# Performance work log

Hardware: AMD Instinct MI355X
Metric: run time of the kernel (lower is better)

Reference implementation:

```python
import jax, jax.numpy as jnp
import numpy as np

B, S, D, F, E, TOP_K = 4, 1024, 512, 2048, 16, 2
TEMPERATURE = 0.5
STD = 0.02


def setup_inputs() -> dict:
    key = jax.random.key(0)
    ks = jax.random.split(key, 9)
    f32 = jnp.float32
    return {
        "x": jax.random.normal(ks[0], (B, S, D), f32),
        # router gate: Linear(D, D//2) -> ReLU -> Linear(D//2, E)
        "gate_w1": jax.random.normal(ks[1], (D, D // 2), f32) * STD,
        "gate_b1": jnp.zeros((D // 2,), f32),
        "gate_w2": jax.random.normal(ks[2], (D // 2, E), f32) * STD,
        "gate_b2": jnp.zeros((E,), f32),
        # stacked expert weights (E experts, each D->F->D)
        "up_w": jax.random.normal(ks[3], (E, D, F), f32) * STD,
        "up_b": jnp.zeros((E, F), f32),
        "down_w": jax.random.normal(ks[4], (E, F, D), f32) * STD,
        "down_b": jnp.zeros((E, D), f32),
    }


def reference(x, gate_w1, gate_b1, gate_w2, gate_b2, up_w, up_b, down_w, down_b):
    num_experts = up_w.shape[0]
    # ---- router ----
    h = jax.nn.relu(x @ gate_w1 + gate_b1)                      # [B,S,D//2]
    scores = h @ gate_w2 + gate_b2                              # [B,S,E]
    routing_probs = jax.nn.softmax(scores / TEMPERATURE, axis=-1)
    # load-balance loss: MSE(mean usage, uniform)
    batch_usage = routing_probs.mean(axis=(0, 1))               # [E]
    load_balance_loss = jnp.mean((batch_usage - 1.0 / num_experts) ** 2)
    # ---- top-k routing weights, renormalized via softmax over selected scores ----
    top_vals, top_idx = jax.lax.top_k(routing_probs, TOP_K)     # [B,S,K]
    top_probs = jax.nn.softmax(top_vals, axis=-1)               # [B,S,K]
    # scatter per-token top-k probs into dense [B,S,E] combine weights
    expert_probs = jnp.einsum(
        "bske,bsk->bse", jax.nn.one_hot(top_idx, num_experts, dtype=x.dtype), top_probs
    )
    # ---- every expert computed densely on all tokens, masked combine (faithful to source) ----
    hid = jax.nn.gelu(
        jnp.einsum("bsd,edf->ebsf", x, up_w) + up_b[:, None, None, :],
        approximate=False,
    )                                                            # [E,B,S,F]
    expert_out = jnp.einsum("ebsf,efd->ebsd", hid, down_w) + down_b[:, None, None, :]
    output = jnp.einsum("ebsd,bse->bsd", expert_out, expert_probs)  # [B,S,D]
    return output, load_balance_loss, routing_probs
```

## Files before the change

### kernel.cpp

```cpp
#include <hip/hip_runtime.h>
#include <hip/hip_bf16.h>

#define NTOK 4096
#define DIM  512
#define DH   256
#define NE   16
#define FF   2048
#define CAP  8192
#define MAXTILES 80
#define TEMP_INV 2.0f

#define OUT_LOSS  (NTOK * DIM)
#define OUT_PROBS (NTOK * DIM + 1)

#define WS_CNT    0
#define WS_USAGE  64
#define WS_NTILES 128
#define WS_DESC   256
#define WS_WTS    1024
#define WS_LISTS  36864
#define WS_HID    (1u << 20)
#define WS_PAIR   (48u << 20)

typedef __attribute__((ext_vector_type(8))) short bf16x8;
typedef __attribute__((ext_vector_type(8))) unsigned short u16x8;
typedef __attribute__((ext_vector_type(4))) float f32x4;

__device__ __forceinline__ unsigned short f2bf(float f) {
  union { float f; unsigned u; } c; c.f = f;
  return (unsigned short)((c.u + 0x7FFFu + ((c.u >> 16) & 1u)) >> 16);
}
__device__ __forceinline__ float gc(const float4& v, int c) {
  return c == 0 ? v.x : c == 1 ? v.y : c == 2 ? v.z : v.w;
}

__launch_bounds__(256)
__global__ void router_kernel(const float* __restrict__ x,
                              const float* __restrict__ w1,
                              const float* __restrict__ b1,
                              const float* __restrict__ w2,
                              const float* __restrict__ b2,
                              float* __restrict__ out,
                              int* __restrict__ cnt,
                              float* __restrict__ usage,
                              float* __restrict__ wts,
                              int* __restrict__ lists) {
  __shared__ __align__(16) float xs[16][DIM];
  __shared__ __align__(16) float hs[16][DH + 4];
  __shared__ __align__(16) float w2s[DH * NE];
  __shared__ float ps[16][NE];

  int tid = threadIdx.x;
  int tok0 = blockIdx.x * 16;

  {
    const float4* xg = (const float4*)(x + (size_t)tok0 * DIM);
    float4* xv = (float4*)&xs[0][0];
    for (int i = tid; i < 16 * DIM / 4; i += 256) xv[i] = xg[i];
    for (int i = tid; i < DH * NE; i += 256) w2s[i] = w2[i];
  }
  __syncthreads();

  {
    int j = tid;
    float acc[16];
    float bj = b1[j];
#pragma unroll
    for (int t = 0; t < 16; ++t) acc[t] = bj;
    for (int k = 0; k < DIM; k += 4) {
      float wa = w1[(k + 0) * DH + j];
      float wb = w1[(k + 1) * DH + j];
      float wcv = w1[(k + 2) * DH + j];
      float wd = w1[(k + 3) * DH + j];
#pragma unroll
      for (int t = 0; t < 16; ++t) {
        float4 xv = *(const float4*)&xs[t][k];
        acc[t] = fmaf(xv.x, wa, acc[t]);
        acc[t] = fmaf(xv.y, wb, acc[t]);
        acc[t] = fmaf(xv.z, wcv, acc[t]);
        acc[t] = fmaf(xv.w, wd, acc[t]);
      }
    }
#pragma unroll
    for (int t = 0; t < 16; ++t) hs[t][j] = fmaxf(acc[t], 0.f);
  }
  __syncthreads();

  int t = tid >> 4, e = tid & 15;
  float s = b2[e];
  for (int j = 0; j < DH; ++j) s = fmaf(hs[t][j], w2s[j * NE + e], s);
  s *= TEMP_INV;
  float m = s;
#pragma unroll
  for (int d = 1; d < 16; d <<= 1) m = fmaxf(m, __shfl_xor(m, d));
  float p = expf(s - m);
  float sum = p;
#pragma unroll
  for (int d = 1; d < 16; d <<= 1) sum += __shfl_xor(sum, d);
  float prob = p / sum;
  out[OUT_PROBS + (size_t)(tok0 + t) * NE + e] = prob;
  ps[t][e] = prob;

  float v = prob;
  v += __shfl_xor(v, 16);
  v += __shfl_xor(v, 32);
  if ((tid & 63) < 16) atomicAdd(&usage[e], v);
  __syncthreads();

  if (tid < 16) {
    int tt = tid;
    float v1 = -1.f; int i1 = 0;
    for (int ee = 0; ee < NE; ++ee) { float pv = ps[tt][ee]; if (pv > v1) { v1 = pv; i1 = ee; } }
    float v2 = -1.f; int i2 = 0;
    for (int ee = 0; ee < NE; ++ee) { if (ee == i1) continue; float pv = ps[tt][ee]; if (pv > v2) { v2 = pv; i2 = ee; } }
    float mm = fmaxf(v1, v2);
    float e0 = expf(v1 - mm), e1 = expf(v2 - mm);
    float rs = 1.f / (e0 + e1);
    int gt = tok0 + tt;
    wts[2 * gt]     = e0 * rs;
    wts[2 * gt + 1] = e1 * rs;
    int p1 = atomicAdd(&cnt[i1], 1);
    lists[i1 * CAP + p1] = 2 * gt;
    int p2 = atomicAdd(&cnt[i2], 1);
    lists[i2 * CAP + p2] = 2 * gt + 1;
  }
}

__global__ void sched_kernel(const int* __restrict__ cnt,
                             const float* __restrict__ usage,
                             int* __restrict__ ntiles,
                             int2* __restrict__ desc,
                             float* __restrict__ out_loss) {
  if (threadIdx.x == 0) {
    int n = 0;
    for (int e = 0; e < NE; ++e) {
      int c = cnt[e];
      for (int i = 0; i < c; i += 128) { desc[n] = make_int2(e, i); ++n; }
    }
    *ntiles = n;
    float loss = 0.f;
    for (int e = 0; e < NE; ++e) {
      float d = usage[e] * (1.f / 4096.f) - (1.f / 16.f);
      loss += d * d;
    }
    *out_loss = loss * (1.f / 16.f);
  }
}

__launch_bounds__(256)
__global__ void up_kernel(const float* __restrict__ x,
                          const float* __restrict__ up_w,
                          const float* __restrict__ up_b,
                          const int* __restrict__ cnt,
                          const int* __restrict__ ntiles,
                          const int2* __restrict__ desc,
                          const int* __restrict__ lists,
                          unsigned short* __restrict__ hid) {
  int ty = blockIdx.y;
  if (ty >= *ntiles) return;
  int2 dd = desc[ty];
  int e = dd.x, i0 = dd.y;
  int cntE = cnt[e];
  int f0 = blockIdx.x * 128;
  const float* __restrict__ W = up_w + (size_t)e * (DIM * FF);

  __shared__ __align__(16) unsigned short As[128 * 64];
  __shared__ __align__(16) unsigned short Bs[128 * 64];

  int tid = threadIdx.x;
  int ar = tid >> 1, ah = tid & 1;
  int aidx = i0 + ar;
  int aslot = (aidx < cntE) ? lists[e * CAP + aidx] : 0;
  const float* __restrict__ xrow = x + (size_t)(aslot >> 1) * DIM;

  int kk8 = tid >> 5;
  int n4 = (tid & 31) << 2;

  int lane = tid & 63, wid = tid >> 6;
  int wr = wid >> 1, wc = wid & 1;
  int ln15 = lane & 15, lq = lane >> 4;

  f32x4 acc[4][4];
#pragma unroll
  for (int i = 0; i < 4; ++i)
#pragma unroll
    for (int j = 0; j < 4; ++j) acc[i][j] = f32x4{0.f, 0.f, 0.f, 0.f};

  for (int ks = 0; ks < DIM / 64; ++ks) {
    int k0 = ks * 64;
#pragma unroll
    for (int i = 0; i < 4; ++i) {
      int g = (ah << 2) + i;
      float4 u = *(const float4*)(xrow + k0 + g * 8);
      float4 w = *(const float4*)(xrow + k0 + g * 8 + 4);
      u16x8 pk;
      pk[0] = f2bf(u.x); pk[1] = f2bf(u.y); pk[2] = f2bf(u.z); pk[3] = f2bf(u.w);
      pk[4] = f2bf(w.x); pk[5] = f2bf(w.y); pk[6] = f2bf(w.z); pk[7] = f2bf(w.w);
      *(u16x8*)(As + ar * 64 + ((g ^ (ar & 7)) << 3)) = pk;
    }
    float4 bw[8];
#pragma unroll
    for (int rr = 0; rr < 8; ++rr)
      bw[rr] = *(const float4*)(W + (size_t)(k0 + kk8 * 8 + rr) * FF + f0 + n4);
#pragma unroll
    for (int c = 0; c < 4; ++c) {
      int n = n4 + c;
      u16x8 pk;
#pragma unroll
      for (int rr = 0; rr < 8; ++rr) pk[rr] = f2bf(gc(bw[rr], c));
      *(u16x8*)(Bs + n * 64 + ((kk8 ^ (n & 7)) << 3)) = pk;
    }
    __syncthreads();
#pragma unroll
    for (int ksub = 0; ksub < 2; ++ksub) {
      bf16x8 a[4], b[4];
      int g = (ksub << 2) + lq;
#pragma unroll
      for (int mi = 0; mi < 4; ++mi) {
        int arow = (wr << 6) + (mi << 4) + ln15;
        a[mi] = *(const bf16x8*)(As + arow * 64 + ((g ^ (arow & 7)) << 3));
      }
#pragma unroll
      for (int ni = 0; ni < 4; ++ni) {
        int bcol = (wc << 6) + (ni << 4) + ln15;
        b[ni] = *(const bf16x8*)(Bs + bcol * 64 + ((g ^ (bcol & 7)) << 3));
      }
#pragma unroll
      for (int mi = 0; mi < 4; ++mi)
#pragma unroll
        for (int ni = 0; ni < 4; ++ni)
          acc[mi][ni] = __builtin_amdgcn_mfma_f32_16x16x32_bf16(a[mi], b[ni], acc[mi][ni], 0, 0, 0);
    }
    __syncthreads();
  }
#pragma unroll
  for (int mi = 0; mi < 4; ++mi) {
    int row_l = (wr << 6) + (mi << 4) + (lq << 2);
#pragma unroll
    for (int ni = 0; ni < 4; ++ni) {
      int col = (wc << 6) + (ni << 4) + ln15;
      float bias = up_b[e * FF + f0 + col];
#pragma unroll
      for (int q = 0; q < 4; ++q) {
        float vv = acc[mi][ni][q] + bias;
        float g = 0.5f * vv * (1.f + erff(vv * 0.70710678118f));
        hid[((size_t)ty * 128 + row_l + q) * FF + f0 + col] = f2bf(g);
      }
    }
  }
}

__launch_bounds__(256)
__global__ void down_kernel(const unsigned short* __restrict__ hid,
                            const float* __restrict__ down_w,
                            const float* __restrict__ down_b,
                            const int* __restrict__ cnt,
                            const int* __restrict__ ntiles,
                            const int2* __restrict__ desc,
                            const int* __restrict__ lists,
                            float* __restrict__ pairbuf) {
  int ty = blockIdx.y;
  if (ty >= *ntiles) return;
  int2 dd = desc[ty];
  int e = dd.x, i0 = dd.y;
  int cntE = cnt[e];
  int n0 = blockIdx.x * 128;
  const float* __restrict__ W = down_w + (size_t)e * (FF * DIM);

  __shared__ __align__(16) unsigned short As[128 * 64];
  __shared__ __align__(16) unsigned short Bs[128 * 64];

  int tid = threadIdx.x;
  int ar = tid >> 1, ah = tid & 1;
  const unsigned short* __restrict__ hrow = hid + ((size_t)ty * 128 + ar) * FF;

  int kk8 = tid >> 5;
  int n4 = (tid & 31) << 2;

  int lane = tid & 63, wid = tid >> 6;
  int wr = wid >> 1, wc = wid & 1;
  int ln15 = lane & 15, lq = lane >> 4;

  f32x4 acc[4][4];
#pragma unroll
  for (int i = 0; i < 4; ++i)
#pragma unroll
    for (int j = 0; j < 4; ++j) acc[i][j] = f32x4{0.f, 0.f, 0.f, 0.f};

  for (int ks = 0; ks < FF / 64; ++ks) {
    int k0 = ks * 64;
#pragma unroll
    for (int i = 0; i < 4; ++i) {
      int g = (ah << 2) + i;
      u16x8 pk = *(const u16x8*)(hrow + k0 + g * 8);
      *(u16x8*)(As + ar * 64 + ((g ^ (ar & 7)) << 3)) = pk;
    }
    float4 bw[8];
#pragma unroll
    for (int rr = 0; rr < 8; ++rr)
      bw[rr] = *(const float4*)(W + (size_t)(k0 + kk8 * 8 + rr) * DIM + n0 + n4);
#pragma unroll
    for (int c = 0; c < 4; ++c) {
      int n = n4 + c;
      u16x8 pk;
#pragma unroll
      for (int rr = 0; rr < 8; ++rr) pk[rr] = f2bf(gc(bw[rr], c));
      *(u16x8*)(Bs + n * 64 + ((kk8 ^ (n & 7)) << 3)) = pk;
    }
    __syncthreads();
#pragma unroll
    for (int ksub = 0; ksub < 2; ++ksub) {
      bf16x8 a[4], b[4];
      int g = (ksub << 2) + lq;
#pragma unroll
      for (int mi = 0; mi < 4; ++mi) {
        int arow = (wr << 6) + (mi << 4) + ln15;
        a[mi] = *(const bf16x8*)(As + arow * 64 + ((g ^ (arow & 7)) << 3));
      }
#pragma unroll
      for (int ni = 0; ni < 4; ++ni) {
        int bcol = (wc << 6) + (ni << 4) + ln15;
        b[ni] = *(const bf16x8*)(Bs + bcol * 64 + ((g ^ (bcol & 7)) << 3));
      }
#pragma unroll
      for (int mi = 0; mi < 4; ++mi)
#pragma unroll
        for (int ni = 0; ni < 4; ++ni)
          acc[mi][ni] = __builtin_amdgcn_mfma_f32_16x16x32_bf16(a[mi], b[ni], acc[mi][ni], 0, 0, 0);
    }
    __syncthreads();
  }
#pragma unroll
  for (int mi = 0; mi < 4; ++mi) {
    int row_l = (wr << 6) + (mi << 4) + (lq << 2);
#pragma unroll
    for (int ni = 0; ni < 4; ++ni) {
      int col = n0 + (wc << 6) + (ni << 4) + ln15;
      float bias = down_b[e * DIM + col];
#pragma unroll
      for (int q = 0; q < 4; ++q) {
        int idx = i0 + row_l + q;
        if (idx < cntE) {
          int slot = lists[e * CAP + idx];
          pairbuf[(size_t)slot * DIM + col] = acc[mi][ni][q] + bias;
        }
      }
    }
  }
}

__launch_bounds__(256)
__global__ void combine_kernel(const float* __restrict__ pairbuf,
                               const float* __restrict__ wts,
                               float* __restrict__ out) {
  int t = blockIdx.x;
  int d = threadIdx.x << 1;
  float w0 = wts[2 * t], w1 = wts[2 * t + 1];
  float2 a = *(const float2*)(pairbuf + (size_t)(2 * t) * DIM + d);
  float2 b = *(const float2*)(pairbuf + (size_t)(2 * t + 1) * DIM + d);
  float2 r; r.x = w0 * a.x + w1 * b.x; r.y = w0 * a.y + w1 * b.y;
  *(float2*)(out + (size_t)t * DIM + d) = r;
}

extern "C" void kernel_launch(void* const* d_in, const int* in_sizes, int n_in,
                              void* d_out, int out_size, void* d_ws, size_t ws_size,
                              hipStream_t stream) {
  (void)in_sizes; (void)n_in; (void)out_size; (void)ws_size;
  const float* x   = (const float*)d_in[0];
  const float* gw1 = (const float*)d_in[1];
  const float* gb1 = (const float*)d_in[2];
  const float* gw2 = (const float*)d_in[3];
  const float* gb2 = (const float*)d_in[4];
  const float* uw  = (const float*)d_in[5];
  const float* ub  = (const float*)d_in[6];
  const float* dw  = (const float*)d_in[7];
  const float* db  = (const float*)d_in[8];
  float* out = (float*)d_out;
  char* ws = (char*)d_ws;

  int*   cnt     = (int*)(ws + WS_CNT);
  float* usage   = (float*)(ws + WS_USAGE);
  int*   ntiles  = (int*)(ws + WS_NTILES);
  int2*  desc    = (int2*)(ws + WS_DESC);
  float* wts     = (float*)(ws + WS_WTS);
  int*   lists   = (int*)(ws + WS_LISTS);
  unsigned short* hid = (unsigned short*)(ws + WS_HID);
  float* pairbuf = (float*)(ws + WS_PAIR);

  hipMemsetAsync(d_ws, 0, 1024, stream);
  router_kernel<<<NTOK / 16, 256, 0, stream>>>(x, gw1, gb1, gw2, gb2, out, cnt, usage, wts, lists);
  sched_kernel<<<1, 64, 0, stream>>>(cnt, usage, ntiles, desc, out + OUT_LOSS);
  up_kernel<<<dim3(FF / 128, MAXTILES), 256, 0, stream>>>(x, uw, ub, cnt, ntiles, desc, lists, hid);
  down_kernel<<<dim3(DIM / 128, MAXTILES), 256, 0, stream>>>(hid, dw, db, cnt, ntiles, desc, lists, pairbuf);
  combine_kernel<<<NTOK, 256, 0, stream>>>(pairbuf, wts, out);
}
```

Baseline: 427.3 us.

## Halve router tokens per block, prefetch gate weights, parallelize scheduler scan

```diff
diff --git a/kernel.cpp b/kernel.cpp
--- a/kernel.cpp
+++ b/kernel.cpp
@@ -9,6 +9,7 @@
 #define CAP  8192
 #define MAXTILES 80
 #define TEMP_INV 2.0f
+#define RTOK 8
 
 #define OUT_LOSS  (NTOK * DIM)
 #define OUT_PROBS (NTOK * DIM + 1)
@@ -45,69 +46,88 @@
                               float* __restrict__ usage,
                               float* __restrict__ wts,
                               int* __restrict__ lists) {
-  __shared__ __align__(16) float xs[16][DIM];
-  __shared__ __align__(16) float hs[16][DH + 4];
+  __shared__ __align__(16) float xs[RTOK][DIM];
+  __shared__ __align__(16) float hs[RTOK][DH + 4];
   __shared__ __align__(16) float w2s[DH * NE];
-  __shared__ float ps[16][NE];
+  __shared__ float ps[RTOK][NE];
+  __shared__ float us[2][NE];
 
   int tid = threadIdx.x;
-  int tok0 = blockIdx.x * 16;
+  int tok0 = blockIdx.x * RTOK;
 
   {
     const float4* xg = (const float4*)(x + (size_t)tok0 * DIM);
     float4* xv = (float4*)&xs[0][0];
-    for (int i = tid; i < 16 * DIM / 4; i += 256) xv[i] = xg[i];
+    for (int i = tid; i < RTOK * DIM / 4; i += 256) xv[i] = xg[i];
     for (int i = tid; i < DH * NE; i += 256) w2s[i] = w2[i];
   }
   __syncthreads();
 
   {
     int j = tid;
-    float acc[16];
+    float acc[RTOK];
     float bj = b1[j];
 #pragma unroll
-    for (int t = 0; t < 16; ++t) acc[t] = bj;
-    for (int k = 0; k < DIM; k += 4) {
-      float wa = w1[(k + 0) * DH + j];
-      float wb = w1[(k + 1) * DH + j];
-      float wcv = w1[(k + 2) * DH + j];
-      float wd = w1[(k + 3) * DH + j];
-#pragma unroll
-      for (int t = 0; t < 16; ++t) {
-        float4 xv = *(const float4*)&xs[t][k];
-        acc[t] = fmaf(xv.x, wa, acc[t]);
-        acc[t] = fmaf(xv.y, wb, acc[t]);
-        acc[t] = fmaf(xv.z, wcv, acc[t]);
-        acc[t] = fmaf(xv.w, wd, acc[t]);
-      }
-    }
-#pragma unroll
-    for (int t = 0; t < 16; ++t) hs[t][j] = fmaxf(acc[t], 0.f);
+    for (int t = 0; t < RTOK; ++t) acc[t] = bj;
+
+    float wq[4][4];
+#pragma unroll
+    for (int g = 0; g < 4; ++g)
+#pragma unroll
+      for (int u = 0; u < 4; ++u)
+        wq[g][u] = w1[(size_t)(g * 4 + u) * DH + j];
+
+#pragma unroll 4
+    for (int g = 0; g < DIM / 4; ++g) {
+      float wcur[4];
+#pragma unroll
+      for (int u = 0; u < 4; ++u) wcur[u] = wq[g & 3][u];
+      int gn = g + 4;
+      if (gn < DIM / 4) {
+#pragma unroll
+        for (int u = 0; u < 4; ++u) wq[g & 3][u] = w1[(size_t)(gn * 4 + u) * DH + j];
+      }
+      int k = g * 4;
+#pragma unroll
+      for (int t = 0; t < RTOK; ++t) {
+        float4 xq = *(const float4*)&xs[t][k];
+        acc[t] = fmaf(xq.x, wcur[0], acc[t]);
+        acc[t] = fmaf(xq.y, wcur[1], acc[t]);
+        acc[t] = fmaf(xq.z, wcur[2], acc[t]);
+        acc[t] = fmaf(xq.w, wcur[3], acc[t]);
+      }
+    }
+#pragma unroll
+    for (int t = 0; t < RTOK; ++t) hs[t][j] = fmaxf(acc[t], 0.f);
   }
   __syncthreads();
 
   int t = tid >> 4, e = tid & 15;
-  float s = b2[e];
-  for (int j = 0; j < DH; ++j) s = fmaf(hs[t][j], w2s[j * NE + e], s);
-  s *= TEMP_INV;
-  float m = s;
-#pragma unroll
-  for (int d = 1; d < 16; d <<= 1) m = fmaxf(m, __shfl_xor(m, d));
-  float p = expf(s - m);
-  float sum = p;
-#pragma unroll
-  for (int d = 1; d < 16; d <<= 1) sum += __shfl_xor(sum, d);
-  float prob = p / sum;
-  out[OUT_PROBS + (size_t)(tok0 + t) * NE + e] = prob;
-  ps[t][e] = prob;
-
-  float v = prob;
-  v += __shfl_xor(v, 16);
-  v += __shfl_xor(v, 32);
-  if ((tid & 63) < 16) atomicAdd(&usage[e], v);
+  if (tid < 128) {
+    float s = b2[e];
+#pragma unroll 8
+    for (int jj = 0; jj < DH; ++jj) s = fmaf(hs[t][jj], w2s[jj * NE + e], s);
+    s *= TEMP_INV;
+    float m = s;
+#pragma unroll
+    for (int d = 1; d < 16; d <<= 1) m = fmaxf(m, __shfl_xor(m, d));
+    float p = expf(s - m);
+    float sum = p;
+#pragma unroll
+    for (int d = 1; d < 16; d <<= 1) sum += __shfl_xor(sum, d);
+    float prob = p / sum;
+    out[OUT_PROBS + (size_t)(tok0 + t) * NE + e] = prob;
+    ps[t][e] = prob;
+
+    float v = prob;
+    v += __shfl_xor(v, 16);
+    v += __shfl_xor(v, 32);
+    if ((tid & 63) < 16) us[tid >> 6][e] = v;
+  }
   __syncthreads();
-
-  if (tid < 16) {
+  if (tid < 16) atomicAdd(&usage[tid], us[0][tid] + us[1][tid]);
+
+  if (tid < RTOK) {
     int tt = tid;
     float v1 = -1.f; int i1 = 0;
     for (int ee = 0; ee < NE; ++ee) { float pv = ps[tt][ee]; if (pv > v1) { v1 = pv; i1 = ee; } }
@@ -131,19 +151,26 @@
                              int* __restrict__ ntiles,
                              int2* __restrict__ desc,
                              float* __restrict__ out_loss) {
-  if (threadIdx.x == 0) {
-    int n = 0;
-    for (int e = 0; e < NE; ++e) {
-      int c = cnt[e];
-      for (int i = 0; i < c; i += 128) { desc[n] = make_int2(e, i); ++n; }
-    }
-    *ntiles = n;
-    float loss = 0.f;
-    for (int e = 0; e < NE; ++e) {
-      float d = usage[e] * (1.f / 4096.f) - (1.f / 16.f);
-      loss += d * d;
-    }
-    *out_loss = loss * (1.f / 16.f);
+  int lane = threadIdx.x;
+  int e = lane & 15;
+  int c = (lane < 16) ? cnt[e] : 0;
+  int tl = (c + 127) >> 7;
+  int v = tl;
+#pragma unroll
+  for (int d = 1; d < 16; d <<= 1) {
+    int u = __shfl_up(v, d);
+    if (lane >= d) v += u;
+  }
+  int excl = v - tl;
+  int tot = __shfl(v, 15);
+  if (lane == 0) *ntiles = tot;
+  if (lane < 16) {
+    for (int i = 0; i < tl; ++i) desc[excl + i] = make_int2(e, i << 7);
+    float d0 = usage[e] * (1.f / 4096.f) - (1.f / 16.f);
+    float ls = d0 * d0;
+#pragma unroll
+    for (int d = 1; d < 16; d <<= 1) ls += __shfl_xor(ls, d);
+    if (lane == 0) *out_loss = ls * (1.f / 16.f);
   }
 }
 
@@ -388,7 +415,7 @@
   float* pairbuf = (float*)(ws + WS_PAIR);
 
   hipMemsetAsync(d_ws, 0, 1024, stream);
-  router_kernel<<<NTOK / 16, 256, 0, stream>>>(x, gw1, gb1, gw2, gb2, out, cnt, usage, wts, lists);
+  router_kernel<<<NTOK / RTOK, 256, 0, stream>>>(x, gw1, gb1, gw2, gb2, out, cnt, usage, wts, lists);
   sched_kernel<<<1, 64, 0, stream>>>(cnt, usage, ntiles, desc, out + OUT_LOSS);
   up_kernel<<<dim3(FF / 128, MAXTILES), 256, 0, stream>>>(x, uw, ub, cnt, ntiles, desc, lists, hid);
   down_kernel<<<dim3(DIM / 128, MAXTILES), 256, 0, stream>>>(hid, dw, db, cnt, ntiles, desc, lists, pairbuf);
```

New measurement: 415.3 us. 1.03x faster.
